# Kernel optimization log

Hardware: AMD Instinct MI355X
Metric: run time of the kernel (lower is better)

## Reference

```python
import jax, jax.numpy as jnp
import numpy as np

B_SZ, SEQ, D_IN, D_HID, D_OUT = 32, 1024, 128, 256, 128
N_FREQ = SEQ // 2 + 1


def setup_inputs() -> dict:
    key = jax.random.key(0)
    ks = jax.random.split(key, 10)
    s_w = 1.0 / np.sqrt(D_IN)
    return {
        "x": jax.random.normal(ks[0], (B_SZ, SEQ, D_IN), dtype=jnp.float32),
        "W_re": jax.random.uniform(ks[1], (N_FREQ, D_IN, D_HID), minval=-s_w, maxval=s_w, dtype=jnp.float32),
        "W_im": jax.random.uniform(ks[2], (N_FREQ, D_IN, D_HID), minval=-s_w, maxval=s_w, dtype=jnp.float32),
        "B_re": jax.random.uniform(ks[3], (N_FREQ, D_HID), minval=-s_w, maxval=s_w, dtype=jnp.float32),
        "B_im": jax.random.uniform(ks[4], (N_FREQ, D_HID), minval=-s_w, maxval=s_w, dtype=jnp.float32),
        "W_rc": jax.random.uniform(ks[5], (D_IN, D_HID), minval=-s_w, maxval=s_w, dtype=jnp.float32),
        "fc1_w": jax.random.uniform(ks[6], (D_HID, D_HID), minval=-1/np.sqrt(D_HID), maxval=1/np.sqrt(D_HID), dtype=jnp.float32),
        "fc1_b": jnp.zeros((D_HID,), dtype=jnp.float32),
        "fc2_w": jax.random.uniform(ks[7], (D_HID, D_OUT), minval=-1/np.sqrt(D_HID), maxval=1/np.sqrt(D_HID), dtype=jnp.float32),
        "fc2_b": jnp.zeros((D_OUT,), dtype=jnp.float32),
    }


def reference(x, W_re, W_im, B_re, B_im, W_rc, fc1_w, fc1_b, fc2_w, fc2_b):
    # residual channel projection: [b,t,d] @ [d,k] -> [b,t,k]
    x_rc = jnp.einsum("btd,dk->btk", x, W_rc)
    # FFT-domain per-frequency complex MLP
    x_fft = jnp.fft.rfft(x, axis=1)  # [b, n_freq, d] complex
    W = W_re + 1j * W_im             # [n_freq, d, k]
    Bc = B_re + 1j * B_im            # [n_freq, k]
    out = jnp.einsum("bti,tio->bto", x_fft, W) + Bc
    # split-ReLU on real/imag parts, recombine as complex
    out = jax.nn.relu(out.real) + 1j * jax.nn.relu(out.imag)
    out = jnp.fft.irfft(out, n=x.shape[1], axis=1)  # [b, t, k] real
    out = out + x_rc
    # 2-layer MLP head with LeakyReLU (slope 0.01)
    h = jax.nn.leaky_relu(out @ fc1_w + fc1_b, negative_slope=0.01)
    return h @ fc2_w + fc2_b
```

## Files before the change

### kernel.cpp

```cpp
#include <hip/hip_runtime.h>
#include <math.h>

#define NB 32
#define NT 1024
#define ND 128
#define NK 256
#define NO 128
#define NF 513

#define PAD(e) ((e) + ((e) >> 4))

typedef __attribute__((ext_vector_type(8))) short bf16x8;
typedef __attribute__((ext_vector_type(4))) float f32x4;

__device__ __forceinline__ unsigned short f2bf(float f) {
  union { float f; unsigned u; } v; v.f = f;
  return (unsigned short)((v.u + 0x7fffu + ((v.u >> 16) & 1u)) >> 16);
}
__device__ __forceinline__ float bf2f(unsigned u) {
  union { unsigned u; float f; } v; v.u = u << 16;
  return v.f;
}
__device__ __forceinline__ unsigned packbf(float re, float im) {
  return (unsigned)f2bf(re) | ((unsigned)f2bf(im) << 16);
}
__device__ __forceinline__ unsigned digrev4(unsigned j) {
  unsigned r = __brev(j) >> 22;
  return ((r & 0x2AAu) >> 1) | ((r & 0x155u) << 1);
}

template <bool INV>
__device__ void fft1024_r4(float* __restrict__ ar, float* __restrict__ ai,
                           const float* __restrict__ twc,
                           const float* __restrict__ tws, int l) {
  for (int j = l; j < 1024; j += 64) {
    int r = (int)digrev4((unsigned)j);
    if (j < r) {
      int pj = PAD(j), pr = PAD(r);
      float t0 = ar[pj], t1 = ai[pj];
      ar[pj] = ar[pr]; ai[pj] = ai[pr];
      ar[pr] = t0; ai[pr] = t1;
    }
  }
#pragma unroll
  for (int s = 0; s < 5; ++s) {
    const int sh = 2 * s;
    const int q = 1 << sh;
#pragma unroll
    for (int it = 0; it < 4; ++it) {
      int m = it * 64 + l;
      int r = m & (q - 1);
      int i0 = ((m >> sh) << (sh + 2)) + r;
      int p0 = PAD(i0), p1 = PAD(i0 + q), p2 = PAD(i0 + 2 * q), p3 = PAD(i0 + 3 * q);
      float x0r = ar[p0], x0i = ai[p0];
      float x1r = ar[p1], x1i = ai[p1];
      float x2r = ar[p2], x2i = ai[p2];
      float x3r = ar[p3], x3i = ai[p3];
      float t1r, t1i, t2r, t2i, t3r, t3i;
      if (s == 0) {
        t1r = x1r; t1i = x1i; t2r = x2r; t2i = x2i; t3r = x3r; t3i = x3i;
      } else {
        int e = r << (8 - sh);
        float c1 = twc[e], s1 = tws[e];
        float c2 = c1 * c1 - s1 * s1, s2 = 2.0f * c1 * s1;
        float c3 = c1 * c2 - s1 * s2, s3 = c1 * s2 + s1 * c2;
        t1r = x1r * c1 - x1i * s1; t1i = x1r * s1 + x1i * c1;
        t2r = x2r * c2 - x2i * s2; t2i = x2r * s2 + x2i * c2;
        t3r = x3r * c3 - x3i * s3; t3i = x3r * s3 + x3i * c3;
      }
      float u0r = x0r + t2r, u0i = x0i + t2i;
      float u1r = x0r - t2r, u1i = x0i - t2i;
      float u2r = t1r + t3r, u2i = t1i + t3i;
      float u3r = t1r - t3r, u3i = t1i - t3i;
      ar[p0] = u0r + u2r; ai[p0] = u0i + u2i;
      ar[p2] = u0r - u2r; ai[p2] = u0i - u2i;
      if (INV) {
        ar[p1] = u1r - u3i; ai[p1] = u1i + u3r;
        ar[p3] = u1r + u3i; ai[p3] = u1i - u3r;
      } else {
        ar[p1] = u1r + u3i; ai[p1] = u1i - u3r;
        ar[p3] = u1r - u3i; ai[p3] = u1i + u3r;
      }
    }
  }
}

__global__ __launch_bounds__(512, 4) void rfft_kernel(const float* __restrict__ x,
                                                      unsigned* __restrict__ Xc) {
  __shared__ float ar[8 * 1088], ai_[8 * 1088];
  __shared__ float twc[768], tws[768];
  const int tid = threadIdx.x;
  const int b = blockIdx.x >> 3;
  const int c0 = (blockIdx.x & 7) << 4;
  for (int k = tid; k < 768; k += 512) {
    float s, c;
    sincosf(6.283185307179586f * (float)k / 1024.0f, &s, &c);
    twc[k] = c; tws[k] = -s;
  }
  const float* xb = x + (size_t)b * NT * ND + c0;
  for (int idx = tid; idx < 8192; idx += 512) {
    int t = idx >> 3, g = idx & 7;
    float2 v = *(const float2*)(xb + (size_t)t * ND + 2 * g);
    int p = g * 1088 + PAD(t);
    ar[p] = v.x; ai_[p] = v.y;
  }
  __syncthreads();
  const int g = tid >> 6, l = tid & 63;
  fft1024_r4<false>(ar + g * 1088, ai_ + g * 1088, twc, tws, l);
  __syncthreads();
  unsigned* Xb = Xc + (size_t)b * NF * ND + c0;
  for (int idx = tid; idx < NF * 8; idx += 512) {
    int f = idx >> 3, gg = idx & 7;
    int mr = (1024 - f) & 1023;
    int pf = gg * 1088 + PAD(f), pm = gg * 1088 + PAD(mr);
    float x1 = ar[pf], y1 = ai_[pf];
    float xr = ar[pm], yr = ai_[pm];
    unsigned e0 = packbf(0.5f * (x1 + xr), 0.5f * (y1 - yr));
    unsigned e1 = packbf(0.5f * (y1 + yr), 0.5f * (xr - x1));
    *(uint2*)(Xb + (size_t)f * ND + 2 * gg) = make_uint2(e0, e1);
  }
}

__global__ __launch_bounds__(512, 4) void freq_mfma_kernel(
    const unsigned* __restrict__ Xc, const float* __restrict__ Wre,
    const float* __restrict__ Wim, const float* __restrict__ Bre,
    const float* __restrict__ Bim, unsigned* __restrict__ Fc) {
  __shared__ unsigned short Xr_l[NB * ND], Xi_l[NB * ND], Xn_l[NB * ND];
  const int tid = threadIdx.x;
  const int f = blockIdx.x >> 1;
  const int nh = blockIdx.x & 1;
#pragma unroll
  for (int it = 0; it < 8; ++it) {
    int idx = it * 512 + tid;
    int d = idx & 127, b = idx >> 7;
    unsigned p = Xc[((size_t)b * NF + f) * ND + d];
    int off = b * 128 + ((((d >> 3) ^ (b & 15))) << 3) + (d & 7);
    unsigned short re = (unsigned short)(p & 0xffff);
    unsigned short im = (unsigned short)(p >> 16);
    Xr_l[off] = re; Xi_l[off] = im; Xn_l[off] = im ^ 0x8000;
  }
  __syncthreads();
  const int wv = tid >> 6, l = tid & 63;
  const int lr = l & 15, lg = l >> 4;
  const int n0 = nh * 128 + wv * 16;
  f32x4 aR[2], aI[2];
  {
    float br = Bre[(size_t)f * NK + n0 + lr];
    float bi = Bim[(size_t)f * NK + n0 + lr];
    aR[0] = (f32x4){br, br, br, br}; aR[1] = aR[0];
    aI[0] = (f32x4){bi, bi, bi, bi}; aI[1] = aI[0];
  }
#pragma unroll
  for (int ks = 0; ks < 4; ++ks) {
    const float* wr = Wre + ((size_t)f * ND + ks * 32 + lg * 8) * NK + n0 + lr;
    const float* wi = Wim + ((size_t)f * ND + ks * 32 + lg * 8) * NK + n0 + lr;
    float fr[8], fi[8];
#pragma unroll
    for (int j = 0; j < 8; ++j) { fr[j] = wr[(size_t)j * NK]; fi[j] = wi[(size_t)j * NK]; }
    bf16x8 xr[2], xi[2], xn[2];
#pragma unroll
    for (int m = 0; m < 2; ++m) {
      int row = m * 16 + lr;
      int off = row * 128 + (((ks * 4 + lg) ^ lr) << 3);
      xr[m] = *(const bf16x8*)&Xr_l[off];
      xi[m] = *(const bf16x8*)&Xi_l[off];
      xn[m] = *(const bf16x8*)&Xn_l[off];
    }
    bf16x8 bR, bI;
#pragma unroll
    for (int j = 0; j < 8; ++j) { bR[j] = (short)f2bf(fr[j]); bI[j] = (short)f2bf(fi[j]); }
#pragma unroll
    for (int m = 0; m < 2; ++m) {
      aR[m] = __builtin_amdgcn_mfma_f32_16x16x32_bf16(xr[m], bR, aR[m], 0, 0, 0);
      aR[m] = __builtin_amdgcn_mfma_f32_16x16x32_bf16(xn[m], bI, aR[m], 0, 0, 0);
      aI[m] = __builtin_amdgcn_mfma_f32_16x16x32_bf16(xr[m], bI, aI[m], 0, 0, 0);
      aI[m] = __builtin_amdgcn_mfma_f32_16x16x32_bf16(xi[m], bR, aI[m], 0, 0, 0);
    }
  }
#pragma unroll
  for (int m = 0; m < 2; ++m)
#pragma unroll
    for (int r = 0; r < 4; ++r) {
      int brow = m * 16 + lg * 4 + r;
      float vR = fmaxf(aR[m][r], 0.0f);
      float vI = fmaxf(aI[m][r], 0.0f);
      Fc[((size_t)brow * NF + f) * NK + n0 + lr] = packbf(vR, vI);
    }
}

__global__ __launch_bounds__(512, 4) void irfft_kernel(const unsigned* __restrict__ Fc,
                                                       unsigned short* __restrict__ yf) {
  __shared__ float ar[8 * 1088], ai_[8 * 1088];
  __shared__ float twc[768], tws[768];
  const int tid = threadIdx.x;
  const int b = blockIdx.x >> 4;
  const int k0 = (blockIdx.x & 15) << 4;
  for (int k = tid; k < 768; k += 512) {
    float s, c;
    sincosf(6.283185307179586f * (float)k / 1024.0f, &s, &c);
    twc[k] = c; tws[k] = s;
  }
  for (int idx = tid; idx < 8192; idx += 512) {
    int f = idx >> 3, g = idx & 7;
    int src = (f <= 512) ? f : 1024 - f;
    uint2 u = *(const uint2*)(Fc + ((size_t)b * NF + src) * NK + k0 + 2 * g);
    float arr = bf2f(u.x & 0xffff), ari = bf2f(u.x >> 16);
    float brr = bf2f(u.y & 0xffff), bri = bf2f(u.y >> 16);
    float zr, zi;
    if (f <= 512) { zr = arr - bri; zi = ari + brr; }
    else          { zr = arr + bri; zi = brr - ari; }
    int p = g * 1088 + PAD(f);
    ar[p] = zr; ai_[p] = zi;
  }
  __syncthreads();
  const int g = tid >> 6, l = tid & 63;
  fft1024_r4<true>(ar + g * 1088, ai_ + g * 1088, twc, tws, l);
  __syncthreads();
  const float sc = 1.0f / 1024.0f;
  unsigned* yb = (unsigned*)(yf + (size_t)b * NT * NK + k0);
  for (int idx = tid; idx < 8192; idx += 512) {
    int t = idx >> 3, gg = idx & 7;
    int p = gg * 1088 + PAD(t);
    yb[(size_t)t * (NK / 2) + gg] = packbf(ar[p] * sc, ai_[p] * sc);
  }
}

__global__ __launch_bounds__(256) void wconv_kernel(const float* __restrict__ Wrc,
                                                    const float* __restrict__ W1,
                                                    const float* __restrict__ W2,
                                                    unsigned short* __restrict__ Wt) {
  int i = blockIdx.x * 256 + threadIdx.x;
  if (i < 32768) {
    int k = i >> 8, n = i & 255;
    Wt[n * 128 + k] = f2bf(Wrc[i]);
  } else if (i < 98304) {
    int j = i - 32768; int k = j >> 8, n = j & 255;
    Wt[32768 + n * 256 + k] = f2bf(W1[j]);
  } else if (i < 131072) {
    int j = i - 98304; int k = j >> 7, n = j & 127;
    Wt[98304 + n * 256 + k] = f2bf(W2[j]);
  }
}

__global__ __launch_bounds__(512, 4) void mlp_fused_kernel(
    const float* __restrict__ x, const unsigned short* __restrict__ yf,
    const unsigned short* __restrict__ Wt, const float* __restrict__ b1,
    const float* __restrict__ b2, float* __restrict__ out) {
  __shared__ unsigned short y_l[64 * 256];
  __shared__ unsigned short u_l[64 * 256];
  const int tid = threadIdx.x;
  const int wv = tid >> 6, l = tid & 63;
  const int lr = l & 15, lg = l >> 4;
  const int row0 = blockIdx.x * 64;
  const unsigned short* W1_t = Wt + 32768;
  const unsigned short* W2_t = Wt + 98304;

#pragma unroll
  for (int it = 0; it < 4; ++it) {
    int idx = it * 512 + tid;
    int row = idx >> 5, c4 = idx & 31;
    float4 v = *(const float4*)(x + (size_t)(row0 + row) * ND + c4 * 4);
    int blk = (c4 >> 1) ^ (row & 15);
    unsigned short* p = &u_l[row * 128 + blk * 8 + (c4 & 1) * 4];
    p[0] = f2bf(v.x); p[1] = f2bf(v.y); p[2] = f2bf(v.z); p[3] = f2bf(v.w);
  }
  __syncthreads();

  f32x4 acc[4][2];
#pragma unroll
  for (int m = 0; m < 4; ++m)
#pragma unroll
    for (int nt = 0; nt < 2; ++nt) acc[m][nt] = (f32x4){0.f, 0.f, 0.f, 0.f};
#pragma unroll
  for (int ks = 0; ks < 4; ++ks) {
    bf16x8 bb[2];
#pragma unroll
    for (int nt = 0; nt < 2; ++nt) {
      int col = wv * 32 + nt * 16 + lr;
      bb[nt] = *(const bf16x8*)&Wt[col * 128 + ks * 32 + lg * 8];
    }
    bf16x8 aa[4];
#pragma unroll
    for (int m = 0; m < 4; ++m) {
      int row = m * 16 + lr;
      aa[m] = *(const bf16x8*)&u_l[row * 128 + (((ks * 4 + lg) ^ (row & 15)) << 3)];
    }
#pragma unroll
    for (int m = 0; m < 4; ++m)
#pragma unroll
      for (int nt = 0; nt < 2; ++nt)
        acc[m][nt] = __builtin_amdgcn_mfma_f32_16x16x32_bf16(aa[m], bb[nt], acc[m][nt], 0, 0, 0);
  }
#pragma unroll
  for (int m = 0; m < 4; ++m)
#pragma unroll
    for (int nt = 0; nt < 2; ++nt)
#pragma unroll
      for (int r = 0; r < 4; ++r) {
        int row = m * 16 + lg * 4 + r;
        int col = wv * 32 + nt * 16 + lr;
        float v = acc[m][nt][r] + bf2f(yf[(size_t)(row0 + row) * NK + col]);
        int blk = (col >> 3) ^ (row & 31);
        y_l[row * 256 + blk * 8 + (col & 7)] = f2bf(v);
      }
  __syncthreads();

  f32x4 a2[4][2];
  {
    float bv0 = b1[wv * 32 + lr], bv1 = b1[wv * 32 + 16 + lr];
#pragma unroll
    for (int m = 0; m < 4; ++m) {
      a2[m][0] = (f32x4){bv0, bv0, bv0, bv0};
      a2[m][1] = (f32x4){bv1, bv1, bv1, bv1};
    }
  }
#pragma unroll
  for (int ks = 0; ks < 8; ++ks) {
    bf16x8 bb[2];
#pragma unroll
    for (int nt = 0; nt < 2; ++nt) {
      int col = wv * 32 + nt * 16 + lr;
      bb[nt] = *(const bf16x8*)&W1_t[col * 256 + ks * 32 + lg * 8];
    }
    bf16x8 aa[4];
#pragma unroll
    for (int m = 0; m < 4; ++m) {
      int row = m * 16 + lr;
      aa[m] = *(const bf16x8*)&y_l[row * 256 + (((ks * 4 + lg) ^ (row & 31)) << 3)];
    }
#pragma unroll
    for (int m = 0; m < 4; ++m)
#pragma unroll
      for (int nt = 0; nt < 2; ++nt)
        a2[m][nt] = __builtin_amdgcn_mfma_f32_16x16x32_bf16(aa[m], bb[nt], a2[m][nt], 0, 0, 0);
  }
#pragma unroll
  for (int m = 0; m < 4; ++m)
#pragma unroll
    for (int nt = 0; nt < 2; ++nt)
#pragma unroll
      for (int r = 0; r < 4; ++r) {
        int row = m * 16 + lg * 4 + r;
        int col = wv * 32 + nt * 16 + lr;
        float v = a2[m][nt][r];
        v = (v > 0.0f) ? v : 0.01f * v;
        int blk = (col >> 3) ^ (row & 31);
        u_l[row * 256 + blk * 8 + (col & 7)] = f2bf(v);
      }
  __syncthreads();

  const int col3 = wv * 16 + lr;
  f32x4 a3[4];
  {
    float bv = b2[col3];
#pragma unroll
    for (int m = 0; m < 4; ++m) a3[m] = (f32x4){bv, bv, bv, bv};
  }
#pragma unroll
  for (int ks = 0; ks < 8; ++ks) {
    bf16x8 bb = *(const bf16x8*)&W2_t[col3 * 256 + ks * 32 + lg * 8];
    bf16x8 aa[4];
#pragma unroll
    for (int m = 0; m < 4; ++m) {
      int row = m * 16 + lr;
      aa[m] = *(const bf16x8*)&u_l[row * 256 + (((ks * 4 + lg) ^ (row & 31)) << 3)];
    }
#pragma unroll
    for (int m = 0; m < 4; ++m)
      a3[m] = __builtin_amdgcn_mfma_f32_16x16x32_bf16(aa[m], bb, a3[m], 0, 0, 0);
  }
#pragma unroll
  for (int m = 0; m < 4; ++m)
#pragma unroll
    for (int r = 0; r < 4; ++r) {
      int row = m * 16 + lg * 4 + r;
      out[(size_t)(row0 + row) * NO + col3] = a3[m][r];
    }
}

extern "C" void kernel_launch(void* const* d_in, const int* in_sizes, int n_in,
                              void* d_out, int out_size, void* d_ws, size_t ws_size,
                              hipStream_t stream) {
  const float* x     = (const float*)d_in[0];
  const float* W_re  = (const float*)d_in[1];
  const float* W_im  = (const float*)d_in[2];
  const float* B_re  = (const float*)d_in[3];
  const float* B_im  = (const float*)d_in[4];
  const float* W_rc  = (const float*)d_in[5];
  const float* fc1_w = (const float*)d_in[6];
  const float* fc1_b = (const float*)d_in[7];
  const float* fc2_w = (const float*)d_in[8];
  const float* fc2_b = (const float*)d_in[9];
  float* out = (float*)d_out;

  const size_t SZ_X = (size_t)NB * NF * ND;
  const size_t SZ_F = (size_t)NB * NF * NK;
  const size_t SZ_Y = (size_t)NB * NT * NK;
  unsigned* Xc = (unsigned*)d_ws;
  unsigned* Fc = Xc + SZ_X;
  unsigned short* yf = (unsigned short*)(Fc + SZ_F);
  unsigned short* Wt = yf + SZ_Y;

  wconv_kernel<<<dim3(512), dim3(256), 0, stream>>>(W_rc, fc1_w, fc2_w, Wt);
  rfft_kernel<<<dim3(NB * 8), dim3(512), 0, stream>>>(x, Xc);
  freq_mfma_kernel<<<dim3(NF * 2), dim3(512), 0, stream>>>(Xc, W_re, W_im, B_re, B_im, Fc);
  irfft_kernel<<<dim3(NB * 16), dim3(512), 0, stream>>>(Fc, yf);
  mlp_fused_kernel<<<dim3((NB * NT) / 64), dim3(512), 0, stream>>>(x, yf, Wt, fc1_b, fc2_b, out);
}
```

Measured before the change: 101.5 us.

## Stage frequency weights through LDS with vectorized loads and finer N split

The per-frequency complex GEMM kernel now loads W_re/W_im with coalesced float4 reads, converts them to bf16 and stores them in swizzled shared memory, instead of each lane issuing strided scalar global loads. The grid is split into four 64-column slices per frequency, with each wave computing a single 16x16 tile. The negated imaginary X copy in LDS is replaced by an in-register sign flip, and X is loaded as uint2 pairs. This targets the weight-streaming cost, which dominates because W is about 270MB of fp32. In exchange it adds more blocks, an extra LDS pass and a changed occupancy hint.

```diff
diff --git a/kernel.cpp b/kernel.cpp
--- a/kernel.cpp
+++ b/kernel.cpp
@@ -121,71 +121,97 @@
   }
 }
 
-__global__ __launch_bounds__(512, 4) void freq_mfma_kernel(
+__global__ __launch_bounds__(512, 6) void freq_mfma_kernel(
     const unsigned* __restrict__ Xc, const float* __restrict__ Wre,
     const float* __restrict__ Wim, const float* __restrict__ Bre,
     const float* __restrict__ Bim, unsigned* __restrict__ Fc) {
-  __shared__ unsigned short Xr_l[NB * ND], Xi_l[NB * ND], Xn_l[NB * ND];
+  __shared__ unsigned short Wr_l[64 * 128], Wi_l[64 * 128];
+  __shared__ unsigned short Xr_l[NB * ND], Xi_l[NB * ND];
   const int tid = threadIdx.x;
-  const int f = blockIdx.x >> 1;
-  const int nh = blockIdx.x & 1;
-#pragma unroll
-  for (int it = 0; it < 8; ++it) {
+  const int f = blockIdx.x >> 2;
+  const int n0 = (blockIdx.x & 3) << 6;
+
+  {
+    const int g = tid >> 4;
+    const int cq = tid & 15;
+    const float* w0 = Wre + (size_t)f * ND * NK + n0 + cq * 4;
+    const float* w1 = Wim + (size_t)f * ND * NK + n0 + cq * 4;
+#pragma unroll
+    for (int w = 0; w < 2; ++w) {
+      const float* wb = w ? w1 : w0;
+      unsigned short* wl = w ? Wi_l : Wr_l;
+      float4 r0 = *(const float4*)(wb + (size_t)(4 * g + 0) * NK);
+      float4 r1 = *(const float4*)(wb + (size_t)(4 * g + 1) * NK);
+      float4 r2 = *(const float4*)(wb + (size_t)(4 * g + 2) * NK);
+      float4 r3 = *(const float4*)(wb + (size_t)(4 * g + 3) * NK);
+      const float* c0 = (const float*)&r0;
+      const float* c1 = (const float*)&r1;
+      const float* c2 = (const float*)&r2;
+      const float* c3 = (const float*)&r3;
+#pragma unroll
+      for (int j = 0; j < 4; ++j) {
+        int nl = cq * 4 + j;
+        int sw = (nl >> 2) ^ ((nl & 3) << 2);
+        int off = nl * 128 + (((g >> 1) ^ sw) << 3) + ((g & 1) << 2);
+        ushort4 v;
+        v.x = f2bf(c0[j]); v.y = f2bf(c1[j]);
+        v.z = f2bf(c2[j]); v.w = f2bf(c3[j]);
+        *(ushort4*)&wl[off] = v;
+      }
+    }
+  }
+#pragma unroll
+  for (int it = 0; it < 4; ++it) {
     int idx = it * 512 + tid;
-    int d = idx & 127, b = idx >> 7;
-    unsigned p = Xc[((size_t)b * NF + f) * ND + d];
-    int off = b * 128 + ((((d >> 3) ^ (b & 15))) << 3) + (d & 7);
-    unsigned short re = (unsigned short)(p & 0xffff);
-    unsigned short im = (unsigned short)(p >> 16);
-    Xr_l[off] = re; Xi_l[off] = im; Xn_l[off] = im ^ 0x8000;
-  }
-  __syncthreads();
+    int bb = idx >> 6, dp = idx & 63;
+    int d = dp * 2;
+    uint2 u = *(const uint2*)(Xc + ((size_t)bb * NF + f) * ND + d);
+    unsigned re2 = (u.x & 0xffffu) | (u.y << 16);
+    unsigned im2 = (u.x >> 16) | (u.y & 0xffff0000u);
+    int off = bb * 128 + ((((d >> 3) ^ (bb & 15))) << 3) + (d & 7);
+    *(unsigned*)&Xr_l[off] = re2;
+    *(unsigned*)&Xi_l[off] = im2;
+  }
+  __syncthreads();
+
   const int wv = tid >> 6, l = tid & 63;
   const int lr = l & 15, lg = l >> 4;
-  const int n0 = nh * 128 + wv * 16;
-  f32x4 aR[2], aI[2];
+  const int wvn = wv & 3, mh = wv >> 2;
+  const int nl = wvn * 16 + lr;
+  const int swn = (nl >> 2) ^ ((nl & 3) << 2);
+  const int row = mh * 16 + lr;
+  f32x4 aR, aI;
   {
-    float br = Bre[(size_t)f * NK + n0 + lr];
-    float bi = Bim[(size_t)f * NK + n0 + lr];
-    aR[0] = (f32x4){br, br, br, br}; aR[1] = aR[0];
-    aI[0] = (f32x4){bi, bi, bi, bi}; aI[1] = aI[0];
+    float br = Bre[(size_t)f * NK + n0 + nl];
+    float bi = Bim[(size_t)f * NK + n0 + nl];
+    aR = (f32x4){br, br, br, br};
+    aI = (f32x4){bi, bi, bi, bi};
   }
 #pragma unroll
   for (int ks = 0; ks < 4; ++ks) {
-    const float* wr = Wre + ((size_t)f * ND + ks * 32 + lg * 8) * NK + n0 + lr;
-    const float* wi = Wim + ((size_t)f * ND + ks * 32 + lg * 8) * NK + n0 + lr;
-    float fr[8], fi[8];
-#pragma unroll
-    for (int j = 0; j < 8; ++j) { fr[j] = wr[(size_t)j * NK]; fi[j] = wi[(size_t)j * NK]; }
-    bf16x8 xr[2], xi[2], xn[2];
-#pragma unroll
-    for (int m = 0; m < 2; ++m) {
-      int row = m * 16 + lr;
-      int off = row * 128 + (((ks * 4 + lg) ^ lr) << 3);
-      xr[m] = *(const bf16x8*)&Xr_l[off];
-      xi[m] = *(const bf16x8*)&Xi_l[off];
-      xn[m] = *(const bf16x8*)&Xn_l[off];
-    }
-    bf16x8 bR, bI;
-#pragma unroll
-    for (int j = 0; j < 8; ++j) { bR[j] = (short)f2bf(fr[j]); bI[j] = (short)f2bf(fi[j]); }
-#pragma unroll
-    for (int m = 0; m < 2; ++m) {
-      aR[m] = __builtin_amdgcn_mfma_f32_16x16x32_bf16(xr[m], bR, aR[m], 0, 0, 0);
-      aR[m] = __builtin_amdgcn_mfma_f32_16x16x32_bf16(xn[m], bI, aR[m], 0, 0, 0);
-      aI[m] = __builtin_amdgcn_mfma_f32_16x16x32_bf16(xr[m], bI, aI[m], 0, 0, 0);
-      aI[m] = __builtin_amdgcn_mfma_f32_16x16x32_bf16(xi[m], bR, aI[m], 0, 0, 0);
-    }
-  }
-#pragma unroll
-  for (int m = 0; m < 2; ++m)
-#pragma unroll
-    for (int r = 0; r < 4; ++r) {
-      int brow = m * 16 + lg * 4 + r;
-      float vR = fmaxf(aR[m][r], 0.0f);
-      float vI = fmaxf(aI[m][r], 0.0f);
-      Fc[((size_t)brow * NF + f) * NK + n0 + lr] = packbf(vR, vI);
-    }
+    int kb = ks * 4 + lg;
+    bf16x8 xr = *(const bf16x8*)&Xr_l[row * 128 + ((kb ^ lr) << 3)];
+    bf16x8 xi = *(const bf16x8*)&Xi_l[row * 128 + ((kb ^ lr) << 3)];
+    bf16x8 bR = *(const bf16x8*)&Wr_l[nl * 128 + ((kb ^ swn) << 3)];
+    bf16x8 bI = *(const bf16x8*)&Wi_l[nl * 128 + ((kb ^ swn) << 3)];
+    union { bf16x8 v; unsigned u[4]; } xiu, xnu;
+    xiu.v = xi;
+    xnu.u[0] = xiu.u[0] ^ 0x80008000u;
+    xnu.u[1] = xiu.u[1] ^ 0x80008000u;
+    xnu.u[2] = xiu.u[2] ^ 0x80008000u;
+    xnu.u[3] = xiu.u[3] ^ 0x80008000u;
+    aR = __builtin_amdgcn_mfma_f32_16x16x32_bf16(xr, bR, aR, 0, 0, 0);
+    aR = __builtin_amdgcn_mfma_f32_16x16x32_bf16(xnu.v, bI, aR, 0, 0, 0);
+    aI = __builtin_amdgcn_mfma_f32_16x16x32_bf16(xr, bI, aI, 0, 0, 0);
+    aI = __builtin_amdgcn_mfma_f32_16x16x32_bf16(xi, bR, aI, 0, 0, 0);
+  }
+#pragma unroll
+  for (int r = 0; r < 4; ++r) {
+    int brow = mh * 16 + lg * 4 + r;
+    float vR = fmaxf(aR[r], 0.0f);
+    float vI = fmaxf(aI[r], 0.0f);
+    Fc[((size_t)brow * NF + f) * NK + n0 + nl] = packbf(vR, vI);
+  }
 }
 
 __global__ __launch_bounds__(512, 4) void irfft_kernel(const unsigned* __restrict__ Fc,
@@ -403,7 +429,7 @@
 
   wconv_kernel<<<dim3(512), dim3(256), 0, stream>>>(W_rc, fc1_w, fc2_w, Wt);
   rfft_kernel<<<dim3(NB * 8), dim3(512), 0, stream>>>(x, Xc);
-  freq_mfma_kernel<<<dim3(NF * 2), dim3(512), 0, stream>>>(Xc, W_re, W_im, B_re, B_im, Fc);
+  freq_mfma_kernel<<<dim3(NF * 4), dim3(512), 0, stream>>>(Xc, W_re, W_im, B_re, B_im, Fc);
   irfft_kernel<<<dim3(NB * 16), dim3(512), 0, stream>>>(Fc, yf);
   mlp_fused_kernel<<<dim3((NB * NT) / 64), dim3(512), 0, stream>>>(x, yf, Wt, fc1_b, fc2_b, out);
 }
```

Result: slower. 103.7 us (+2.2%).

## Stage per-frequency weights through LDS with coalesced float4 loads, one block per frequency

Applied to the files above, without the earlier changes.

The per-frequency complex matmul kernel now uses one block per frequency instead of two. Each block loads the full W_re/W_im slice with coalesced float4 global reads, converts it to bf16 and stores it in swizzled LDS. The old path did strided scalar weight loads per lane. Each wave now computes a 32x32 output tile, and the negated imaginary X is made in registers instead of being stored in LDS. The cost is about 160KB of LDS per block, which limits occupancy, and half as many blocks in the grid.

```diff
diff --git a/kernel.cpp b/kernel.cpp
--- a/kernel.cpp
+++ b/kernel.cpp
@@ -9,6 +9,7 @@
 #define NF 513
 
 #define PAD(e) ((e) + ((e) >> 4))
+#define FSW(n) ((((n) >> 2) & 15) ^ (((n) & 3) << 2))
 
 typedef __attribute__((ext_vector_type(8))) short bf16x8;
 typedef __attribute__((ext_vector_type(4))) float f32x4;
@@ -121,71 +122,149 @@
   }
 }
 
-__global__ __launch_bounds__(512, 4) void freq_mfma_kernel(
+__global__ __launch_bounds__(512, 2) void freq_mfma_kernel(
     const unsigned* __restrict__ Xc, const float* __restrict__ Wre,
     const float* __restrict__ Wim, const float* __restrict__ Bre,
     const float* __restrict__ Bim, unsigned* __restrict__ Fc) {
-  __shared__ unsigned short Xr_l[NB * ND], Xi_l[NB * ND], Xn_l[NB * ND];
+  __shared__ unsigned short Wr_l[NK * 128];
+  __shared__ unsigned short Wi_l[NK * 128];
+  __shared__ unsigned short Xr_l[NB * ND], Xi_l[NB * ND];
   const int tid = threadIdx.x;
-  const int f = blockIdx.x >> 1;
-  const int nh = blockIdx.x & 1;
-#pragma unroll
-  for (int it = 0; it < 8; ++it) {
+  const int f = blockIdx.x;
+  const int rt0 = tid >> 6;
+  const int ct = tid & 63;
+
+  const float* pre = Wre + (size_t)f * ND * NK;
+  const float* pim = Wim + (size_t)f * ND * NK;
+  float4 wr[16], wi[16];
+#pragma unroll
+  for (int c = 0; c < 4; ++c) {
+    int rt = rt0 + 8 * c;
+#pragma unroll
+    for (int r = 0; r < 4; ++r)
+      wr[c * 4 + r] = *(const float4*)(pre + (size_t)(4 * rt + r) * NK + 4 * ct);
+  }
+#pragma unroll
+  for (int c = 0; c < 4; ++c) {
+    int rt = rt0 + 8 * c;
+#pragma unroll
+    for (int r = 0; r < 4; ++r)
+      wi[c * 4 + r] = *(const float4*)(pim + (size_t)(4 * rt + r) * NK + 4 * ct);
+  }
+  uint2 xs[4];
+#pragma unroll
+  for (int it = 0; it < 4; ++it) {
     int idx = it * 512 + tid;
-    int d = idx & 127, b = idx >> 7;
-    unsigned p = Xc[((size_t)b * NF + f) * ND + d];
-    int off = b * 128 + ((((d >> 3) ^ (b & 15))) << 3) + (d & 7);
-    unsigned short re = (unsigned short)(p & 0xffff);
-    unsigned short im = (unsigned short)(p >> 16);
-    Xr_l[off] = re; Xi_l[off] = im; Xn_l[off] = im ^ 0x8000;
-  }
-  __syncthreads();
-  const int wv = tid >> 6, l = tid & 63;
-  const int lr = l & 15, lg = l >> 4;
-  const int n0 = nh * 128 + wv * 16;
-  f32x4 aR[2], aI[2];
-  {
-    float br = Bre[(size_t)f * NK + n0 + lr];
-    float bi = Bim[(size_t)f * NK + n0 + lr];
-    aR[0] = (f32x4){br, br, br, br}; aR[1] = aR[0];
-    aI[0] = (f32x4){bi, bi, bi, bi}; aI[1] = aI[0];
+    int bb = idx >> 6, dp = idx & 63;
+    xs[it] = *(const uint2*)(Xc + ((size_t)bb * NF + f) * ND + 2 * dp);
+  }
+
+#pragma unroll
+  for (int c = 0; c < 4; ++c) {
+    int rt = rt0 + 8 * c;
+    int ib = rt >> 1, hf = rt & 1;
+    const float* q0 = (const float*)&wr[c * 4 + 0];
+    const float* q1 = (const float*)&wr[c * 4 + 1];
+    const float* q2 = (const float*)&wr[c * 4 + 2];
+    const float* q3 = (const float*)&wr[c * 4 + 3];
+#pragma unroll
+    for (int j = 0; j < 4; ++j) {
+      int n = 4 * ct + j;
+      int off = n * 128 + ((ib ^ FSW(n)) << 3) + (hf << 2);
+      ushort4 v;
+      v.x = f2bf(q0[j]); v.y = f2bf(q1[j]); v.z = f2bf(q2[j]); v.w = f2bf(q3[j]);
+      *(ushort4*)&Wr_l[off] = v;
+    }
+  }
+#pragma unroll
+  for (int c = 0; c < 4; ++c) {
+    int rt = rt0 + 8 * c;
+    int ib = rt >> 1, hf = rt & 1;
+    const float* q0 = (const float*)&wi[c * 4 + 0];
+    const float* q1 = (const float*)&wi[c * 4 + 1];
+    const float* q2 = (const float*)&wi[c * 4 + 2];
+    const float* q3 = (const float*)&wi[c * 4 + 3];
+#pragma unroll
+    for (int j = 0; j < 4; ++j) {
+      int n = 4 * ct + j;
+      int off = n * 128 + ((ib ^ FSW(n)) << 3) + (hf << 2);
+      ushort4 v;
+      v.x = f2bf(q0[j]); v.y = f2bf(q1[j]); v.z = f2bf(q2[j]); v.w = f2bf(q3[j]);
+      *(ushort4*)&Wi_l[off] = v;
+    }
+  }
+#pragma unroll
+  for (int it = 0; it < 4; ++it) {
+    int idx = it * 512 + tid;
+    int bb = idx >> 6, dp = idx & 63;
+    int d = 2 * dp;
+    uint2 u = xs[it];
+    unsigned re2 = (u.x & 0xffffu) | (u.y << 16);
+    unsigned im2 = (u.x >> 16) | (u.y & 0xffff0000u);
+    int off = bb * 128 + ((((d >> 3) ^ (bb & 15))) << 3) + (d & 7);
+    *(unsigned*)&Xr_l[off] = re2;
+    *(unsigned*)&Xi_l[off] = im2;
+  }
+  __syncthreads();
+
+  const int lr = tid & 15, lg = (tid & 63) >> 4;
+  const int nb = rt0 * 32;
+  f32x4 aR[2][2], aI[2][2];
+#pragma unroll
+  for (int nt = 0; nt < 2; ++nt) {
+    float br = Bre[(size_t)f * NK + nb + nt * 16 + lr];
+    float bi = Bim[(size_t)f * NK + nb + nt * 16 + lr];
+#pragma unroll
+    for (int mh = 0; mh < 2; ++mh) {
+      aR[mh][nt] = (f32x4){br, br, br, br};
+      aI[mh][nt] = (f32x4){bi, bi, bi, bi};
+    }
   }
 #pragma unroll
   for (int ks = 0; ks < 4; ++ks) {
-    const float* wr = Wre + ((size_t)f * ND + ks * 32 + lg * 8) * NK + n0 + lr;
-    const float* wi = Wim + ((size_t)f * ND + ks * 32 + lg * 8) * NK + n0 + lr;
-    float fr[8], fi[8];
-#pragma unroll
-    for (int j = 0; j < 8; ++j) { fr[j] = wr[(size_t)j * NK]; fi[j] = wi[(size_t)j * NK]; }
-    bf16x8 xr[2], xi[2], xn[2];
-#pragma unroll
-    for (int m = 0; m < 2; ++m) {
-      int row = m * 16 + lr;
-      int off = row * 128 + (((ks * 4 + lg) ^ lr) << 3);
-      xr[m] = *(const bf16x8*)&Xr_l[off];
-      xi[m] = *(const bf16x8*)&Xi_l[off];
-      xn[m] = *(const bf16x8*)&Xn_l[off];
-    }
-    bf16x8 bR, bI;
-#pragma unroll
-    for (int j = 0; j < 8; ++j) { bR[j] = (short)f2bf(fr[j]); bI[j] = (short)f2bf(fi[j]); }
-#pragma unroll
-    for (int m = 0; m < 2; ++m) {
-      aR[m] = __builtin_amdgcn_mfma_f32_16x16x32_bf16(xr[m], bR, aR[m], 0, 0, 0);
-      aR[m] = __builtin_amdgcn_mfma_f32_16x16x32_bf16(xn[m], bI, aR[m], 0, 0, 0);
-      aI[m] = __builtin_amdgcn_mfma_f32_16x16x32_bf16(xr[m], bI, aI[m], 0, 0, 0);
-      aI[m] = __builtin_amdgcn_mfma_f32_16x16x32_bf16(xi[m], bR, aI[m], 0, 0, 0);
-    }
-  }
-#pragma unroll
-  for (int m = 0; m < 2; ++m)
-#pragma unroll
-    for (int r = 0; r < 4; ++r) {
-      int brow = m * 16 + lg * 4 + r;
-      float vR = fmaxf(aR[m][r], 0.0f);
-      float vI = fmaxf(aI[m][r], 0.0f);
-      Fc[((size_t)brow * NF + f) * NK + n0 + lr] = packbf(vR, vI);
-    }
+    int kb = ks * 4 + lg;
+    bf16x8 xr[2], xi2[2], xn[2];
+#pragma unroll
+    for (int mh = 0; mh < 2; ++mh) {
+      int row = mh * 16 + lr;
+      int xoff = row * 128 + ((kb ^ lr) << 3);
+      xr[mh] = *(const bf16x8*)&Xr_l[xoff];
+      xi2[mh] = *(const bf16x8*)&Xi_l[xoff];
+      union { bf16x8 v; unsigned u[4]; } a, b;
+      a.v = xi2[mh];
+      b.u[0] = a.u[0] ^ 0x80008000u;
+      b.u[1] = a.u[1] ^ 0x80008000u;
+      b.u[2] = a.u[2] ^ 0x80008000u;
+      b.u[3] = a.u[3] ^ 0x80008000u;
+      xn[mh] = b.v;
+    }
+#pragma unroll
+    for (int nt = 0; nt < 2; ++nt) {
+      int nl = nb + nt * 16 + lr;
+      int woff = nl * 128 + ((kb ^ FSW(nl)) << 3);
+      bf16x8 bR = *(const bf16x8*)&Wr_l[woff];
+      bf16x8 bI = *(const bf16x8*)&Wi_l[woff];
+#pragma unroll
+      for (int mh = 0; mh < 2; ++mh) {
+        aR[mh][nt] = __builtin_amdgcn_mfma_f32_16x16x32_bf16(xr[mh], bR, aR[mh][nt], 0, 0, 0);
+        aR[mh][nt] = __builtin_amdgcn_mfma_f32_16x16x32_bf16(xn[mh], bI, aR[mh][nt], 0, 0, 0);
+        aI[mh][nt] = __builtin_amdgcn_mfma_f32_16x16x32_bf16(xr[mh], bI, aI[mh][nt], 0, 0, 0);
+        aI[mh][nt] = __builtin_amdgcn_mfma_f32_16x16x32_bf16(xi2[mh], bR, aI[mh][nt], 0, 0, 0);
+      }
+    }
+  }
+#pragma unroll
+  for (int mh = 0; mh < 2; ++mh)
+#pragma unroll
+    for (int nt = 0; nt < 2; ++nt)
+#pragma unroll
+      for (int r = 0; r < 4; ++r) {
+        int brow = mh * 16 + lg * 4 + r;
+        int col = nb + nt * 16 + lr;
+        float vR = fmaxf(aR[mh][nt][r], 0.0f);
+        float vI = fmaxf(aI[mh][nt][r], 0.0f);
+        Fc[((size_t)brow * NF + f) * NK + col] = packbf(vR, vI);
+      }
 }
 
 __global__ __launch_bounds__(512, 4) void irfft_kernel(const unsigned* __restrict__ Fc,
@@ -403,7 +482,7 @@
 
   wconv_kernel<<<dim3(512), dim3(256), 0, stream>>>(W_rc, fc1_w, fc2_w, Wt);
   rfft_kernel<<<dim3(NB * 8), dim3(512), 0, stream>>>(x, Xc);
-  freq_mfma_kernel<<<dim3(NF * 2), dim3(512), 0, stream>>>(Xc, W_re, W_im, B_re, B_im, Fc);
+  freq_mfma_kernel<<<dim3(NF), dim3(512), 0, stream>>>(Xc, W_re, W_im, B_re, B_im, Fc);
   irfft_kernel<<<dim3(NB * 16), dim3(512), 0, stream>>>(Fc, yf);
   mlp_fused_kernel<<<dim3((NB * NT) / 64), dim3(512), 0, stream>>>(x, yf, Wt, fc1_b, fc2_b, out);
 }
```

After: 104.9 us. 3.4% more time.
